# Kernel tuning notes

Hardware: AMD Instinct MI355X
Metric: run time of the kernel (lower is better)

## Reference

```python
import jax, jax.numpy as jnp
import numpy as np

# ---- hardcoded module constants (from Cyborg.__init__) ----
B, S, V = 256, 128, 512
H = 30              # number of symbol vectors
N_STACKS = 2
R = 2               # REDUNDANCY
DEPTH = 4           # stack_depth
ZERO_OFFSET = 1e-6
NAND_BIAS = 3.0
INIT_SHARPEN = 10.0
N_VECS = 1 + N_STACKS  # input vec + one peek per stack = 3
C_BIG = (H + N_STACKS) * R   # 64 choices for push_fn / calc_out
C_SMALL = 2 * R              # 4 choices for pop_op / push_op


def _cossim(a, b, eps=1e-8):
    # torch.cosine_similarity semantics: per-vector norm clamp
    na = jnp.maximum(jnp.linalg.norm(a, axis=-1, keepdims=True), eps)
    nb = jnp.maximum(jnp.linalg.norm(b, axis=-1, keepdims=True), eps)
    return jnp.sum((a / na) * (b / nb), axis=-1)


def _nand(query, w, nw_raw):
    # Fuzzy-NAND gate bank (neurallambda NAND, clip='abs').
    # query: [B, N_VECS*V], w: [C, N_VECS*V], nw_raw: [C, N_VECS] -> [B, C]
    C = w.shape[0]
    q = query.reshape(-1, 1, N_VECS, V)
    wv = w.reshape(1, C, N_VECS, V)
    cos = jnp.abs(_cossim(q, wv))                 # [B, C, N_VECS], clip='abs'
    nw = jax.nn.sigmoid(nw_raw)[None]             # interpolate sim vs NOT(sim)
    interp = nw * cos + (1.0 - nw) * (1.0 - cos)
    return jnp.prod(interp, axis=-1)              # fuzzy AND over the 3 vecs


# ---- differentiable stack (soft pointer over DEPTH slots) ----
def _read(stack, ptr):
    return jnp.einsum('bdv,bd->bv', stack, ptr)

def _push(stack, ptr, val):
    p = jnp.roll(ptr, 1, axis=1)
    s = stack * (1.0 - p)[..., None] + val[:, None, :] * p[..., None]
    return s, p

def _pop(stack, ptr):
    s = stack * (1.0 - ptr)[..., None] + ZERO_OFFSET * ptr[..., None]
    p = jnp.roll(ptr, -1, axis=1)
    return s, p

def _pop_or_nop(stack, ptr, sharp, should_pop, should_nop):
    pr = jax.nn.softmax(jnp.stack([should_pop, should_nop], -1) * sharp, axis=-1)
    ps, pp = _pop(stack, ptr)
    s = ps * pr[:, 0, None, None] + stack * pr[:, 1, None, None]
    p = pp * pr[:, 0, None] + ptr * pr[:, 1, None]
    return s, p

def _push_or_nop(stack, ptr, sharp, should_push, should_nop, val):
    pr = jax.nn.softmax(jnp.stack([should_push, should_nop], -1) * sharp, axis=-1)
    ps, pp = _push(stack, ptr, val)
    s = ps * pr[:, 0, None, None] + stack * pr[:, 1, None, None]
    p = pp * pr[:, 0, None] + ptr * pr[:, 1, None]
    return s, p


def _forward(x, syms, stack_init_vec, sharp, pop_w, pop_nw, pushop_w, pushop_nw,
             pushfn_w, pushfn_nw, calc_w, calc_nw):
    b = x.shape[0]
    # init both stacks to zero_offset, pointer at slot 0, then hard-push init vec
    stack0 = jnp.full((N_STACKS, b, DEPTH, V), ZERO_OFFSET, x.dtype)
    ptr0 = jnp.zeros((N_STACKS, b, DEPTH), x.dtype).at[:, :, 0].set(1.0)
    init_val = jnp.broadcast_to(stack_init_vec, (b, V))
    stack0, ptr0 = jax.vmap(_push, in_axes=(0, 0, None))(stack0, ptr0, init_val)

    syms_b = jnp.broadcast_to(syms, (b, H, V))

    def step(carry, inp):
        stacks, ptrs = carry                                    # [2,B,D,V], [2,B,D]
        peeks = jax.vmap(_read)(stacks, ptrs)                   # [2,B,V]
        inps = jnp.concatenate([inp, peeks[0], peeks[1]], -1)   # [B,3V]
        out_opts = jnp.concatenate(
            [syms_b, peeks[0][:, None], peeks[1][:, None]], 1)  # [B,H+2,V]
        new_s, new_p = [], []
        for k in range(N_STACKS):
            pops = _nand(inps, pop_w[k], pop_nw[k])             # [B, 2R]
            pushes = _nand(inps, pushop_w[k], pushop_nw[k])     # [B, 2R]
            pv = _nand(inps, pushfn_w[k], pushfn_nw[k]).reshape(b, H + N_STACKS, R)
            push_val = jnp.einsum('bcv,bcr->bv', out_opts, pv)
            s, p = _pop_or_nop(stacks[k], ptrs[k], sharp[k],
                               pops[:, :R].max(1), pops[:, R:].max(1))
            s, p = _push_or_nop(s, p, sharp[k],
                                pushes[:, :R].max(1), pushes[:, R:].max(1), push_val)
            new_s.append(s)
            new_p.append(p)
        stacks = jnp.stack(new_s)
        ptrs = jnp.stack(new_p)
        peeks2 = jax.vmap(_read)(stacks, ptrs)
        inps2 = jnp.concatenate([inp, peeks2[0], peeks2[1]], -1)
        out_opts2 = jnp.concatenate(
            [syms_b, peeks2[0][:, None], peeks2[1][:, None]], 1)
        cv = _nand(inps2, calc_w, calc_nw).reshape(b, H + N_STACKS, R)
        out = jnp.einsum('bcv,bcr->bv', out_opts2, cv)
        return (stacks, ptrs), out

    _, outs = jax.lax.scan(step, (stack0, ptr0), jnp.swapaxes(x, 0, 1))
    return jnp.swapaxes(outs, 0, 1)  # [B,S,V]


def setup_inputs() -> dict:
    key = jax.random.key(0)
    ks = jax.random.split(key, 12)
    siv = jax.random.normal(ks[1], (V,), jnp.float32)
    siv = siv / jnp.linalg.norm(siv)
    return {
        'x': jax.random.normal(ks[0], (B, S, V), jnp.float32),
        'syms': jax.random.normal(ks[2], (H, V), jnp.float32),
        'stack_init_vec': siv,
        'sharp': jnp.full((N_STACKS,), INIT_SHARPEN, jnp.float32),
        'pop_w': jax.random.normal(ks[3], (N_STACKS, C_SMALL, N_VECS * V), jnp.float32),
        'pop_nw': jax.random.normal(ks[4], (N_STACKS, C_SMALL, N_VECS), jnp.float32) + NAND_BIAS,
        'pushop_w': jax.random.normal(ks[5], (N_STACKS, C_SMALL, N_VECS * V), jnp.float32),
        'pushop_nw': jax.random.normal(ks[6], (N_STACKS, C_SMALL, N_VECS), jnp.float32) + NAND_BIAS,
        'pushfn_w': jax.random.normal(ks[7], (N_STACKS, C_BIG, N_VECS * V), jnp.float32),
        'pushfn_nw': jax.random.normal(ks[8], (N_STACKS, C_BIG, N_VECS), jnp.float32) + NAND_BIAS,
        'calc_w': jax.random.normal(ks[9], (C_BIG, N_VECS * V), jnp.float32),
        'calc_nw': jax.random.normal(ks[10], (C_BIG, N_VECS), jnp.float32) + NAND_BIAS,
    }


def reference(x, syms, stack_init_vec, sharp, pop_w, pop_nw, pushop_w, pushop_nw,
              pushfn_w, pushfn_nw, calc_w, calc_nw):
    return _forward(x, syms, stack_init_vec, sharp, pop_w, pop_nw, pushop_w,
                    pushop_nw, pushfn_w, pushfn_nw, calc_w, calc_nw)
```

## Files before the change

kernel.cpp:

```cpp
#include <hip/hip_runtime.h>
#include <math.h>


#define SS 128
#define VV 512
#define NROWS 208
#define ZOFF 1e-6f

#define OFF_I0   0
#define OFF_OC   (32768*208)
#define OFF_GI   (OFF_OC + 32768*32)
#define OFF_M    (OFF_GI + 2*32*208)
#define OFF_A    (OFF_M + 1024)
#define OFF_Bc   (OFF_A + 624)
#define OFF_W0   (OFF_Bc + 624)

typedef _Float16 half8 __attribute__((ext_vector_type(8)));
typedef float f32x4 __attribute__((ext_vector_type(4)));

__device__ __forceinline__ float rlane(float v, int lane) {
    return __int_as_float(__builtin_amdgcn_readlane(__float_as_int(v), lane));
}
template <int CTRL>
__device__ __forceinline__ float dpp_add(float x) {
    int y = __builtin_amdgcn_update_dpp(0, __float_as_int(x), CTRL, 0xF, 0xF, true);
    return x + __int_as_float(y);
}
__device__ __forceinline__ float sum16(float x) {
    x = dpp_add<0xB1>(x);
    x = dpp_add<0x4E>(x);
    x = dpp_add<0x124>(x);
    x = dpp_add<0x128>(x);
    return x;
}
__device__ __forceinline__ float swz16(float x) {
    return __int_as_float(__builtin_amdgcn_ds_swizzle(__float_as_int(x), 0x401F));
}

__device__ __forceinline__ const float* w_row(int r, const float* pw, const float* pow_,
                                              const float* pfw, const float* cw) {
    if (r < 8)   return pw   + r * 1536;
    if (r < 16)  return pow_ + (r - 8) * 1536;
    if (r < 144) return pfw  + (r - 16) * 1536;
    return cw + (r - 144) * 1536;
}
__device__ __forceinline__ const float* nw_row(int r, const float* pn, const float* pon,
                                               const float* pfn, const float* cn) {
    if (r < 8)   return pn   + r * 3;
    if (r < 16)  return pon  + (r - 8) * 3;
    if (r < 144) return pfn  + (r - 16) * 3;
    return cn + (r - 144) * 3;
}

__global__ void kB(const float* __restrict__ syms, const float* __restrict__ siv,
                   const float* __restrict__ pw, const float* __restrict__ pn,
                   const float* __restrict__ pow_, const float* __restrict__ pon,
                   const float* __restrict__ pfw, const float* __restrict__ pfn,
                   const float* __restrict__ cw, const float* __restrict__ cn,
                   float* __restrict__ ws) {
    int blk = blockIdx.x, tid = threadIdx.x;
    if (blk < 64) {
        int jj = blk >> 5, e = blk & 31;
        __shared__ float bas[512];
        for (int i = tid; i < 512; i += 256)
            bas[i] = (e == 0) ? 1.0f : ((e == 1) ? siv[i] : syms[(e - 2) * 512 + i]);
        __syncthreads();
        if (tid < NROWS) {
            int c = tid;
            const float4* w4 = (const float4*)(w_row(c, pw, pow_, pfw, cw) + (jj + 1) * 512);
            const float4* b4 = (const float4*)bas;
            float s = 0.f;
            for (int q = 0; q < 128; ++q) {
                float4 a = b4[q], b = w4[q];
                s += a.x * b.x + a.y * b.y + a.z * b.z + a.w * b.w;
            }
            ws[OFF_GI + (jj * 32 + e) * 208 + c] = s;
        }
    } else if (blk == 64) {
        __shared__ float basw[32 * 512];
        for (int i = tid; i < 32 * 512; i += 256) {
            int m = i >> 9, v = i & 511;
            basw[i] = (m == 0) ? 1.0f : ((m == 1) ? siv[v] : syms[(m - 2) * 512 + v]);
        }
        __syncthreads();
        for (int p = tid; p < 1024; p += 256) {
            int m = p >> 5, mm = p & 31;
            const float4* a4 = (const float4*)(basw + m * 512);
            const float4* b4 = (const float4*)(basw + mm * 512);
            float s = 0.f;
            for (int q = 0; q < 128; ++q) {
                float4 a = a4[q], b = b4[q];
                s += a.x * b.x + a.y * b.y + a.z * b.z + a.w * b.w;
            }
            ws[OFF_M + p] = s;
        }
    } else if (blk == 65) {
        for (int idx = tid; idx < 624; idx += 256) {
            int r = idx / 3, j = idx % 3;
            const float4* w4 = (const float4*)(w_row(r, pw, pow_, pfw, cw) + j * 512);
            float s = 0.f;
            for (int q = 0; q < 128; ++q) {
                float4 b = w4[q];
                s += b.x * b.x + b.y * b.y + b.z * b.z + b.w * b.w;
            }
            float nrm = fmaxf(sqrtf(s), 1e-8f);
            float nwv = nw_row(r, pn, pon, pfn, cn)[j];
            float sig = 1.f / (1.f + expf(-nwv));
            ws[OFF_A + idx]  = (2.f * sig - 1.f) / nrm;
            ws[OFF_Bc + idx] = 1.f - sig;
        }
    } else {
        int part = blk - 66;
        _Float16* whp = (_Float16*)(ws + OFF_W0);
        _Float16* wlp = whp + 208 * 512;
        for (int i = tid; i < 6656; i += 256) {
            int flat = part * 6656 + i;
            int c = flat >> 9, v = flat & 511;
            float wv = w_row(c, pw, pow_, pfw, cw)[v];
            _Float16 h = (_Float16)wv;
            whp[flat] = h;
            wlp[flat] = (_Float16)(wv - (float)h);
        }
    }
}

__global__ __launch_bounds__(256) void kA(const float* __restrict__ x, float* __restrict__ ws) {
    __shared__ half8 AH[2][256];
    __shared__ half8 AL[2][256];
    __shared__ float red[256];
    __shared__ float invx[64];
    const int tid = threadIdx.x;
    const int wid = tid >> 6, l = tid & 63;
    const size_t bt0 = (size_t)blockIdx.x * 64;

    const int sr = tid >> 2, ss = tid & 3;
    const float* xp = x + (bt0 + sr) * 512 + ss * 8;
    const int wpos = (sr >> 4) * 64 + (sr & 15) + (ss << 4);

    const _Float16* whp = (const _Float16*)(ws + OFF_W0);
    const _Float16* wlp = whp + 208 * 512;

    const int t0 = (wid == 0) ? 0 : (1 + 3 * wid);
    const int nt = (wid == 0) ? 4 : 3;

    f32x4 acc[4][4];
#pragma unroll
    for (int m = 0; m < 4; ++m)
#pragma unroll
        for (int tt = 0; tt < 4; ++tt)
            acc[m][tt] = (f32x4){0.f, 0.f, 0.f, 0.f};

    float sumsq = 0.f;
    auto stage = [&](int kt, int buf) {
        float v[8];
        *(float4*)v       = *(const float4*)(xp + kt * 32);
        *(float4*)(v + 4) = *(const float4*)(xp + kt * 32 + 4);
        half8 hh, hl;
#pragma unroll
        for (int j = 0; j < 8; ++j) {
            sumsq += v[j] * v[j];
            _Float16 h = (_Float16)v[j];
            hh[j] = h;
            hl[j] = (_Float16)(v[j] - (float)h);
        }
        AH[buf][wpos] = hh;
        AL[buf][wpos] = hl;
    };

    stage(0, 0);
    __syncthreads();

    for (int kt = 0; kt < 16; ++kt) {
        const int buf = kt & 1;
        if (kt < 15) stage(kt + 1, buf ^ 1);

        half8 ahm[4], alm[4];
#pragma unroll
        for (int m = 0; m < 4; ++m) {
            ahm[m] = AH[buf][m * 64 + l];
            alm[m] = AL[buf][m * 64 + l];
        }
        const int kof = kt * 32 + (l >> 4) * 8;
#pragma unroll
        for (int tt = 0; tt < 4; ++tt) {
            if (tt < nt) {
                const int c = (t0 + tt) * 16 + (l & 15);
                half8 bh = *(const half8*)(whp + c * 512 + kof);
                half8 bl = *(const half8*)(wlp + c * 512 + kof);
#pragma unroll
                for (int m = 0; m < 4; ++m) {
                    acc[m][tt] = __builtin_amdgcn_mfma_f32_16x16x32_f16(ahm[m], bh, acc[m][tt], 0, 0, 0);
                    acc[m][tt] = __builtin_amdgcn_mfma_f32_16x16x32_f16(ahm[m], bl, acc[m][tt], 0, 0, 0);
                    acc[m][tt] = __builtin_amdgcn_mfma_f32_16x16x32_f16(alm[m], bh, acc[m][tt], 0, 0, 0);
                }
            }
        }
        __syncthreads();
    }

    red[tid] = sumsq;
    __syncthreads();
    if (tid < 64) {
        float s = red[tid * 4] + red[tid * 4 + 1] + red[tid * 4 + 2] + red[tid * 4 + 3];
        invx[tid] = 1.f / fmaxf(sqrtf(s), 1e-8f);
    }
    __syncthreads();

#pragma unroll
    for (int tt = 0; tt < 4; ++tt) {
        if (tt < nt) {
            const int c = (t0 + tt) * 16 + (l & 15);
            const float A0 = ws[OFF_A + c * 3];
            const float B0 = ws[OFF_Bc + c * 3];
#pragma unroll
            for (int m = 0; m < 4; ++m) {
                const int rbase = m * 16 + (l >> 4) * 4;
#pragma unroll
                for (int j = 0; j < 4; ++j) {
                    const float ix = invx[rbase + j];
                    ws[OFF_I0 + (bt0 + rbase + j) * 208 + c] = A0 * fabsf(acc[m][tt][j]) * ix + B0;
                }
            }
        }
    }
}

__global__ __attribute__((amdgpu_flat_work_group_size(256, 256), amdgpu_waves_per_eu(1, 1)))
void kC(float* __restrict__ ws, const float* __restrict__ sharp) {
    __shared__ float pkL[64];
    __shared__ float nndL[2][144];
    const int b = blockIdx.x, tid = threadIdx.x;
    const int wid = tid >> 6, l = tid & 63;
    const int k = l >> 5, m = l & 31;
    const int isW3 = (wid == 3);
    const int isRow = (tid < 144);
    const int r = isW3 ? (144 + l) : tid;

    const float* GI = ws + OFF_GI;
    float G[64];
#pragma unroll
    for (int i = 0; i < 32; ++i) {
        G[i]      = GI[i * 208 + r];
        G[32 + i] = GI[(32 + i) * 208 + r];
    }
    const float A1 = ws[OFF_A + r * 3 + 1],  A2 = ws[OFF_A + r * 3 + 2];
    const float B1 = ws[OFF_Bc + r * 3 + 1], B2 = ws[OFF_Bc + r * 3 + 2];
    float4 Mr[8];
#pragma unroll
    for (int q = 0; q < 8; ++q) Mr[q] = *(const float4*)(ws + OFF_M + m * 32 + 4 * q);
    const float sh = sharp[k];

    float st[4], p[4];
#pragma unroll
    for (int d = 0; d < 4; ++d) {
        st[d] = (d == 1) ? ((m == 1) ? 1.f : 0.f) : ((m == 0) ? ZOFF : 0.f);
        p[d] = (d == 1) ? 1.f : 0.f;
    }
    float pk = st[0] * p[0] + st[1] * p[1] + st[2] * p[2] + st[3] * p[3];
    float pkOther = __shfl_xor(pk, 32);

    const float* i0base = ws + OFF_I0 + (size_t)b * SS * 208;
    const int ioff = isW3 ? 0 : 1;
    float i0pro = i0base[r];
    float i0use = i0base[(size_t)ioff * 208 + r];

    auto CA = [&](float pp, float po, float iv) -> float {
        float gq0[2] = {0.f, 0.f}, gq1[2] = {0.f, 0.f};
        float d1[2] = {0.f, 0.f}, d2[2] = {0.f, 0.f};
#pragma unroll
        for (int q = 0; q < 8; ++q) {
            float4 aq = *(const float4*)(pkL + 4 * q);
            float4 cq = *(const float4*)(pkL + 32 + 4 * q);
            float4 mq = Mr[q];
            gq0[q & 1] += mq.x * aq.x + mq.y * aq.y + mq.z * aq.z + mq.w * aq.w;
            gq1[q & 1] += mq.x * cq.x + mq.y * cq.y + mq.z * cq.z + mq.w * cq.w;
            d1[q & 1]  += aq.x * G[4*q]   + aq.y * G[4*q+1]   + aq.z * G[4*q+2]   + aq.w * G[4*q+3];
            d2[q & 1]  += cq.x * G[32+4*q] + cq.y * G[33+4*q] + cq.z * G[34+4*q] + cq.w * G[35+4*q];
        }
        float pm0 = (k ? po : pp) * (gq0[0] + gq0[1]);
        float pm1 = (k ? pp : po) * (gq1[0] + gq1[1]);
        float q0 = sum16(pm0); q0 += swz16(q0);
        float q1 = sum16(pm1); q1 += swz16(q1);
        float iq0 = __frsqrt_rn(fmaxf(q0, 1e-16f));
        float iq1 = __frsqrt_rn(fmaxf(q1, 1e-16f));
        float dd1 = d1[0] + d1[1], dd2 = d2[0] + d2[1];
        return iv * (A1 * fabsf(dd1) * iq0 + B1) * (A2 * fabsf(dd2) * iq1 + B2);
    };

    if (wid == 0) pkL[l] = pk;
    __syncthreads();
    {
        float nv0 = CA(pk, pkOther, i0pro);
        if (isRow) nndL[0][tid] = nv0;
    }
    __syncthreads();

    for (int t = 0; t < SS; ++t) {
        int nidx = t + 1 + ioff; if (nidx > SS - 1) nidx = SS - 1;
        float i0nxt = i0base[(size_t)nidx * 208 + r];

        const float* nb = nndL[t & 1];
        float4 gp4 = *(const float4*)(nb + 4 * k);
        float4 gq4 = *(const float4*)(nb + 8 + 4 * k);
        float prp0 = 1.f / (1.f + __expf((fmaxf(gp4.z, gp4.w) - fmaxf(gp4.x, gp4.y)) * sh));
        float prq0 = 1.f / (1.f + __expf((fmaxf(gq4.z, gq4.w) - fmaxf(gq4.x, gq4.y)) * sh));
        float prp1 = 1.f - prp0, prq1 = 1.f - prq0;
        float prx = 0.f, pry = 0.f;
        if (m >= 2) {
            float2 pr2 = *(const float2*)(nb + 16 + 64 * k + 2 * m - 4);
            prx = pr2.x; pry = pr2.y;
        }
        float4 t30 = *(const float4*)(nb + 16 + 64 * k + 60);
        float pk0m = k ? pkOther : pk;
        float pk1m = k ? pk : pkOther;
        float pvc = prx + pry + (t30.x + t30.y) * pk0m + (t30.z + t30.w) * pk1m;

        float zc = (m == 0) ? ZOFF : 0.f;
        float s1[4], p1[4];
#pragma unroll
        for (int d = 0; d < 4; ++d) {
            float ps = st[d] * (1.f - p[d]) + zc * p[d];
            s1[d] = ps * prp0 + st[d] * prp1;
            p1[d] = p[(d + 1) & 3] * prp0 + p[d] * prp1;
        }
#pragma unroll
        for (int d = 0; d < 4; ++d) {
            float pu = p1[(d + 3) & 3];
            float su = s1[d] * (1.f - pu) + pvc * pu;
            st[d] = su * prq0 + s1[d] * prq1;
            p[d] = pu * prq0 + p1[d] * prq1;
        }
        float pkp = st[0] * p[0] + st[1] * p[1] + st[2] * p[2] + st[3] * p[3];
        float pkpOth = __shfl_xor(pkp, 32);
        if (wid == 0) pkL[l] = pkp;
        __syncthreads();

        float nv = CA(pkp, pkpOth, i0use);
        if (isRow) nndL[(t + 1) & 1][tid] = nv;
        if (isW3) {
            float s60 = rlane(nv, 60), s61 = rlane(nv, 61);
            float s62 = rlane(nv, 62), s63 = rlane(nv, 63);
            int src = (m >= 2) ? (2 * m - 4) : 0;
            float cx = __shfl(nv, src);
            float cy = __shfl(nv, src + 1);
            if (m < 2) { cx = 0.f; cy = 0.f; }
            if (l < 32) {
                float oc = cx + cy + (s60 + s61) * pkp + (s62 + s63) * pkpOth;
                ws[OFF_OC + ((size_t)b * SS + t) * 32 + m] = oc;
            }
        }
        __syncthreads();
        pk = pkp;
        pkOther = pkpOth;
        i0use = i0nxt;
    }
}

__global__ __launch_bounds__(256) void kD(const float* __restrict__ ws, const float* __restrict__ syms,
                                          const float* __restrict__ siv, float* __restrict__ out) {
    int t = threadIdx.x;
    int rg = t >> 6;
    int vc = (t & 63) * 8;
    size_t r0 = (size_t)blockIdx.x * 16 + rg * 4;
    const float* oc = ws + OFF_OC;
    float acc[4][8];
    float4 sv0 = *(const float4*)(siv + vc);
    float4 sv1 = *(const float4*)(siv + vc + 4);
#pragma unroll
    for (int rr = 0; rr < 4; ++rr) {
        float c0 = oc[(r0 + rr) * 32 + 0];
        float c1 = oc[(r0 + rr) * 32 + 1];
        acc[rr][0] = c0 + c1 * sv0.x; acc[rr][1] = c0 + c1 * sv0.y;
        acc[rr][2] = c0 + c1 * sv0.z; acc[rr][3] = c0 + c1 * sv0.w;
        acc[rr][4] = c0 + c1 * sv1.x; acc[rr][5] = c0 + c1 * sv1.y;
        acc[rr][6] = c0 + c1 * sv1.z; acc[rr][7] = c0 + c1 * sv1.w;
    }
    for (int mm = 0; mm < 30; ++mm) {
        float4 b0 = *(const float4*)(syms + mm * 512 + vc);
        float4 b1 = *(const float4*)(syms + mm * 512 + vc + 4);
#pragma unroll
        for (int rr = 0; rr < 4; ++rr) {
            float c = oc[(r0 + rr) * 32 + 2 + mm];
            acc[rr][0] += c * b0.x; acc[rr][1] += c * b0.y;
            acc[rr][2] += c * b0.z; acc[rr][3] += c * b0.w;
            acc[rr][4] += c * b1.x; acc[rr][5] += c * b1.y;
            acc[rr][6] += c * b1.z; acc[rr][7] += c * b1.w;
        }
    }
#pragma unroll
    for (int rr = 0; rr < 4; ++rr) {
        float* o = out + (r0 + rr) * 512 + vc;
        *(float4*)o       = make_float4(acc[rr][0], acc[rr][1], acc[rr][2], acc[rr][3]);
        *(float4*)(o + 4) = make_float4(acc[rr][4], acc[rr][5], acc[rr][6], acc[rr][7]);
    }
}

extern "C" void kernel_launch(void* const* d_in, const int* in_sizes, int n_in,
                              void* d_out, int out_size, void* d_ws, size_t ws_size,
                              hipStream_t stream) {
    const float* x    = (const float*)d_in[0];
    const float* syms = (const float*)d_in[1];
    const float* siv  = (const float*)d_in[2];
    const float* shp  = (const float*)d_in[3];
    const float* pw   = (const float*)d_in[4];
    const float* pn   = (const float*)d_in[5];
    const float* pow_ = (const float*)d_in[6];
    const float* pon  = (const float*)d_in[7];
    const float* pfw  = (const float*)d_in[8];
    const float* pfn  = (const float*)d_in[9];
    const float* cw   = (const float*)d_in[10];
    const float* cn   = (const float*)d_in[11];
    float* ws  = (float*)d_ws;
    float* out = (float*)d_out;

    hipLaunchKernelGGL(kB, dim3(82),   dim3(256), 0, stream,
                       syms, siv, pw, pn, pow_, pon, pfw, pfn, cw, cn, ws);
    hipLaunchKernelGGL(kA, dim3(512),  dim3(256), 0, stream, x, ws);
    hipLaunchKernelGGL(kC, dim3(256),  dim3(256), 0, stream, ws, shp);
    hipLaunchKernelGGL(kD, dim3(2048), dim3(256), 0, stream, ws, syms, siv, out);
}
```

Before: 405.0 us.

## Broadcast stack peek via readlane instead of LDS, reorder GEMM staging loads

In the sequential recurrence kernel, the per-step peek vector is no longer written to shared memory and re-read behind a barrier. Each wave instead reads it from its own lanes with readlane broadcasts, which removes one __syncthreads per timestep. This relies on every wave computing the same stack state redundantly. In the GEMM kernel, the next tile's global loads are issued before the MFMA loop and converted and stored to LDS after it, so load latency overlaps compute.

```diff
diff --git a/kernel.cpp b/kernel.cpp
--- a/kernel.cpp
+++ b/kernel.cpp
@@ -151,10 +151,11 @@
             acc[m][tt] = (f32x4){0.f, 0.f, 0.f, 0.f};
 
     float sumsq = 0.f;
-    auto stage = [&](int kt, int buf) {
+
+    {
         float v[8];
-        *(float4*)v       = *(const float4*)(xp + kt * 32);
-        *(float4*)(v + 4) = *(const float4*)(xp + kt * 32 + 4);
+        *(float4*)v       = *(const float4*)(xp);
+        *(float4*)(v + 4) = *(const float4*)(xp + 4);
         half8 hh, hl;
 #pragma unroll
         for (int j = 0; j < 8; ++j) {
@@ -163,22 +164,23 @@
             hh[j] = h;
             hl[j] = (_Float16)(v[j] - (float)h);
         }
-        AH[buf][wpos] = hh;
-        AL[buf][wpos] = hl;
-    };
-
-    stage(0, 0);
+        AH[0][wpos] = hh;
+        AL[0][wpos] = hl;
+    }
     __syncthreads();
 
     for (int kt = 0; kt < 16; ++kt) {
         const int buf = kt & 1;
-        if (kt < 15) stage(kt + 1, buf ^ 1);
-
         half8 ahm[4], alm[4];
 #pragma unroll
         for (int m = 0; m < 4; ++m) {
             ahm[m] = AH[buf][m * 64 + l];
             alm[m] = AL[buf][m * 64 + l];
+        }
+        float4 xv0, xv1;
+        if (kt < 15) {
+            xv0 = *(const float4*)(xp + (kt + 1) * 32);
+            xv1 = *(const float4*)(xp + (kt + 1) * 32 + 4);
         }
         const int kof = kt * 32 + (l >> 4) * 8;
 #pragma unroll
@@ -195,6 +197,20 @@
                 }
             }
         }
+        if (kt < 15) {
+            float v[8];
+            *(float4*)v = xv0; *(float4*)(v + 4) = xv1;
+            half8 hh, hl;
+#pragma unroll
+            for (int j = 0; j < 8; ++j) {
+                sumsq += v[j] * v[j];
+                _Float16 h = (_Float16)v[j];
+                hh[j] = h;
+                hl[j] = (_Float16)(v[j] - (float)h);
+            }
+            AH[buf ^ 1][wpos] = hh;
+            AL[buf ^ 1][wpos] = hl;
+        }
         __syncthreads();
     }
 
@@ -227,7 +243,6 @@
 
 __global__ __attribute__((amdgpu_flat_work_group_size(256, 256), amdgpu_waves_per_eu(1, 1)))
 void kC(float* __restrict__ ws, const float* __restrict__ sharp) {
-    __shared__ float pkL[64];
     __shared__ float nndL[2][144];
     const int b = blockIdx.x, tid = threadIdx.x;
     const int wid = tid >> 6, l = tid & 63;
@@ -245,9 +260,12 @@
     }
     const float A1 = ws[OFF_A + r * 3 + 1],  A2 = ws[OFF_A + r * 3 + 2];
     const float B1 = ws[OFF_Bc + r * 3 + 1], B2 = ws[OFF_Bc + r * 3 + 2];
-    float4 Mr[8];
-#pragma unroll
-    for (int q = 0; q < 8; ++q) Mr[q] = *(const float4*)(ws + OFF_M + m * 32 + 4 * q);
+    float Mrow[32];
+#pragma unroll
+    for (int q = 0; q < 8; ++q) {
+        float4 mr = *(const float4*)(ws + OFF_M + m * 32 + 4 * q);
+        Mrow[4*q] = mr.x; Mrow[4*q+1] = mr.y; Mrow[4*q+2] = mr.z; Mrow[4*q+3] = mr.w;
+    }
     const float sh = sharp[k];
 
     float st[4], p[4];
@@ -265,30 +283,30 @@
     float i0use = i0base[(size_t)ioff * 208 + r];
 
     auto CA = [&](float pp, float po, float iv) -> float {
-        float gq0[2] = {0.f, 0.f}, gq1[2] = {0.f, 0.f};
-        float d1[2] = {0.f, 0.f}, d2[2] = {0.f, 0.f};
-#pragma unroll
-        for (int q = 0; q < 8; ++q) {
-            float4 aq = *(const float4*)(pkL + 4 * q);
-            float4 cq = *(const float4*)(pkL + 32 + 4 * q);
-            float4 mq = Mr[q];
-            gq0[q & 1] += mq.x * aq.x + mq.y * aq.y + mq.z * aq.z + mq.w * aq.w;
-            gq1[q & 1] += mq.x * cq.x + mq.y * cq.y + mq.z * cq.z + mq.w * cq.w;
-            d1[q & 1]  += aq.x * G[4*q]   + aq.y * G[4*q+1]   + aq.z * G[4*q+2]   + aq.w * G[4*q+3];
-            d2[q & 1]  += cq.x * G[32+4*q] + cq.y * G[33+4*q] + cq.z * G[34+4*q] + cq.w * G[35+4*q];
-        }
-        float pm0 = (k ? po : pp) * (gq0[0] + gq0[1]);
-        float pm1 = (k ? pp : po) * (gq1[0] + gq1[1]);
+        float gq0a = 0.f, gq0b = 0.f, gq1a = 0.f, gq1b = 0.f;
+        float d1a = 0.f, d1b = 0.f, d2a = 0.f, d2b = 0.f;
+#pragma unroll
+        for (int mm = 0; mm < 32; ++mm) {
+            float v0 = rlane(pp, mm);
+            float v1 = rlane(pp, 32 + mm);
+            if (mm & 1) {
+                gq0b += Mrow[mm] * v0;  gq1b += Mrow[mm] * v1;
+                d1b  += G[mm] * v0;     d2b  += G[32 + mm] * v1;
+            } else {
+                gq0a += Mrow[mm] * v0;  gq1a += Mrow[mm] * v1;
+                d1a  += G[mm] * v0;     d2a  += G[32 + mm] * v1;
+            }
+        }
+        float pm0 = (k ? po : pp) * (gq0a + gq0b);
+        float pm1 = (k ? pp : po) * (gq1a + gq1b);
         float q0 = sum16(pm0); q0 += swz16(q0);
         float q1 = sum16(pm1); q1 += swz16(q1);
         float iq0 = __frsqrt_rn(fmaxf(q0, 1e-16f));
         float iq1 = __frsqrt_rn(fmaxf(q1, 1e-16f));
-        float dd1 = d1[0] + d1[1], dd2 = d2[0] + d2[1];
+        float dd1 = d1a + d1b, dd2 = d2a + d2b;
         return iv * (A1 * fabsf(dd1) * iq0 + B1) * (A2 * fabsf(dd2) * iq1 + B2);
     };
 
-    if (wid == 0) pkL[l] = pk;
-    __syncthreads();
     {
         float nv0 = CA(pk, pkOther, i0pro);
         if (isRow) nndL[0][tid] = nv0;
@@ -332,8 +350,6 @@
         }
         float pkp = st[0] * p[0] + st[1] * p[1] + st[2] * p[2] + st[3] * p[3];
         float pkpOth = __shfl_xor(pkp, 32);
-        if (wid == 0) pkL[l] = pkp;
-        __syncthreads();
 
         float nv = CA(pkp, pkpOth, i0use);
         if (isRow) nndL[(t + 1) & 1][tid] = nv;
```

After: 384.6 us. 5.0% less time.
